# Kernel optimization log

Hardware: AMD Instinct MI355X
Metric: run time of the kernel (lower is better)

## Reference

```python
import jax, jax.numpy as jnp
import numpy as np

N_EMBD = 1024
N_EXPERTS = 8
TOP_K = 2
D_FF = 4 * N_EMBD


def setup_inputs() -> dict:
    key = jax.random.key(0)
    ks = jax.random.split(key, 7)
    s_in = 1.0 / np.sqrt(N_EMBD)
    s_ff = 1.0 / np.sqrt(D_FF)
    return {
        "x": jax.random.normal(ks[0], (2, 2048, N_EMBD), dtype=jnp.float32),
        "Wr": jax.random.normal(ks[1], (N_EMBD, N_EXPERTS), dtype=jnp.float32) * s_in,
        "br": jnp.zeros((N_EXPERTS,), dtype=jnp.float32),
        "W1": jax.random.normal(ks[2], (N_EXPERTS, N_EMBD, D_FF), dtype=jnp.float32) * s_in,
        "b1": jnp.zeros((N_EXPERTS, D_FF), dtype=jnp.float32),
        "W2": jax.random.normal(ks[3], (N_EXPERTS, D_FF, N_EMBD), dtype=jnp.float32) * s_ff,
        "b2": jnp.zeros((N_EXPERTS, N_EMBD), dtype=jnp.float32),
    }


def _moe_forward(x, Wr, br, W1, b1, W2, b2):
    b, t, e = x.shape
    flat_x = x.reshape(-1, e)                      # [T, d]
    T = flat_x.shape[0]
    # --- TopKRouter: logits -> top_k -> sparse softmax over selected experts ---
    logits = flat_x @ Wr + br                      # [T, E]
    top_vals, top_idx = jax.lax.top_k(logits, TOP_K)
    neg_inf = jnp.full_like(logits, -jnp.inf)
    masked = neg_inf.at[jnp.arange(T)[:, None], top_idx].set(top_vals)
    probs = jax.nn.softmax(masked, axis=-1)        # [T, E], zeros outside top-k
    # --- Per-expert FFN, weighted combine (dense weights make this a sum) ---
    out = jnp.zeros_like(flat_x)
    for ei in range(N_EXPERTS):
        h = jax.nn.relu(flat_x @ W1[ei] + b1[ei])  # [T, 4d]
        y = h @ W2[ei] + b2[ei]                    # [T, d]
        out = out + probs[:, ei:ei + 1] * y
    return out.reshape(b, t, e)


def reference(x, Wr, br, W1, b1, W2, b2):
    return _moe_forward(x, Wr, br, W1, b1, W2, b2)
```

## Files before the change

kernel.cpp:

```cpp
#include <hip/hip_runtime.h>
#include <cstdio>
#include <cstdint>

#define TOKS 4096
#define DMODEL 1024
#define DFF 4096
#define NEXP 8

typedef __bf16 bf16_8 __attribute__((ext_vector_type(8)));
typedef float f32x4 __attribute__((ext_vector_type(4)));
typedef __attribute__((address_space(1))) const void* gptr_t;
typedef __attribute__((address_space(3))) void* lptr_t;

__device__ __forceinline__ unsigned short f2bf(float f) {
  unsigned int u = __builtin_bit_cast(unsigned int, f);
  u += 0x7FFFu + ((u >> 16) & 1u);
  return (unsigned short)(u >> 16);
}

__global__ __launch_bounds__(256) void transpose_cast_k(const float* __restrict__ in,
                                                        unsigned short* __restrict__ out,
                                                        int R, int C) {
  __shared__ float tile[64][65];
  const float* inm = in + (size_t)blockIdx.y * R * C;
  unsigned short* outm = out + (size_t)blockIdx.y * R * C;
  int tcn = C >> 6;
  int tr = blockIdx.x / tcn, tc = blockIdx.x % tcn;
  int r0 = tr << 6, c0 = tc << 6;
  int tid = threadIdx.x;
  int lr = tid >> 6, lc = tid & 63;
#pragma unroll
  for (int i = 0; i < 16; ++i)
    tile[lr + 4 * i][lc] = inm[(size_t)(r0 + lr + 4 * i) * C + c0 + lc];
  __syncthreads();
#pragma unroll
  for (int i = 0; i < 8; ++i) {
    int row = (tid >> 5) + i * 8;
    int colu = tid & 31;
    float f0 = tile[colu * 2][row];
    float f1 = tile[colu * 2 + 1][row];
    unsigned int u = (unsigned int)f2bf(f0) | ((unsigned int)f2bf(f1) << 16);
    *(unsigned int*)(outm + (size_t)(c0 + row) * R + r0 + colu * 2) = u;
  }
}

__global__ __launch_bounds__(256) void cast_x_k(const float* __restrict__ x,
                                                unsigned short* __restrict__ xb) {
  int i = blockIdx.x * 256 + threadIdx.x;
  float4 f = ((const float4*)x)[i];
  ushort4 u;
  u.x = f2bf(f.x); u.y = f2bf(f.y); u.z = f2bf(f.z); u.w = f2bf(f.w);
  ((ushort4*)xb)[i] = u;
}

__global__ __launch_bounds__(256) void router_k(const float* __restrict__ x,
                                                const float* __restrict__ Wr,
                                                const float* __restrict__ br,
                                                int* __restrict__ cnt,
                                                int* __restrict__ list,
                                                float* __restrict__ plist) {
  int t = blockIdx.x * 4 + (threadIdx.x >> 6);
  int lane = threadIdx.x & 63;
  float a[NEXP];
#pragma unroll
  for (int e = 0; e < NEXP; ++e) a[e] = 0.f;
  const float* xr = x + (size_t)t * DMODEL;
  for (int i = lane; i < DMODEL; i += 64) {
    float xv = xr[i];
    const float* wr = Wr + (size_t)i * NEXP;
#pragma unroll
    for (int e = 0; e < NEXP; ++e) a[e] += xv * wr[e];
  }
#pragma unroll
  for (int off = 32; off > 0; off >>= 1) {
#pragma unroll
    for (int e = 0; e < NEXP; ++e) a[e] += __shfl_xor(a[e], off);
  }
  if (lane == 0) {
#pragma unroll
    for (int e = 0; e < NEXP; ++e) a[e] += br[e];
    int i0 = 0; float m0 = a[0];
#pragma unroll
    for (int e = 1; e < NEXP; ++e) if (a[e] > m0) { m0 = a[e]; i0 = e; }
    int i1 = -1; float m1 = -1e30f;
#pragma unroll
    for (int e = 0; e < NEXP; ++e) if (e != i0 && a[e] > m1) { m1 = a[e]; i1 = e; }
    float tt = expf(m1 - m0);
    float p0 = 1.f / (1.f + tt);
    float p1 = 1.f - p0;
    int pos0 = atomicAdd(&cnt[i0], 1);
    list[i0 * TOKS + pos0] = t; plist[i0 * TOKS + pos0] = p0;
    int pos1 = atomicAdd(&cnt[i1], 1);
    list[i1 * TOKS + pos1] = t; plist[i1 * TOKS + pos1] = p1;
  }
}

__global__ void offsets_k(const int* __restrict__ cnt, int* __restrict__ off) {
  if (threadIdx.x == 0) {
    int s = 0;
    for (int e = 0; e < NEXP; ++e) { off[e] = s; s += cnt[e]; }
    off[NEXP] = s;
  }
}

template <int MODE, int BM, int BN>
__global__ __launch_bounds__(512, 2) void moe_gemm_k(
    const unsigned short* __restrict__ Abase, const unsigned short* __restrict__ Bbase,
    const float* __restrict__ bias, const int* __restrict__ cnt, const int* __restrict__ off,
    const int* __restrict__ list, const float* __restrict__ plist,
    unsigned short* __restrict__ Hout, float* __restrict__ Out) {
  constexpr int K  = (MODE == 0) ? DMODEL : DFF;
  constexpr int NN = (MODE == 0) ? DFF : DMODEL;
  constexpr int NT = NN / BN;
  constexpr int MT = TOKS / BM;
  constexpr int NWG = NEXP * MT * NT;
  constexpr int CHUNK = NWG / 8;
  constexpr int WMSZ = BM / 2;
  constexpr int WNSZ = BN / 4;
  constexpr int FM = WMSZ / 16;
  constexpr int FN = WNSZ / 16;
  constexpr int RA = BM / 64;
  constexpr int RB = BN / 64;

  const int flat = blockIdx.x + NT * (blockIdx.y + MT * blockIdx.z);
  const int u = (flat & 7) * CHUNK + (flat >> 3);
  const int nt = u % NT;
  const int mt = (u / NT) % MT;
  const int e = u / (NT * MT);

  const int ce = cnt[e];
  const int m0 = mt * BM;
  if (m0 >= ce) return;
  const int rem = ce - m0;
  const int n0 = nt * BN;
  const int oe = off[e];

  __shared__ unsigned short As[2][BM * 64];
  __shared__ unsigned short Bs[2][BN * 64];

  const int tid = threadIdx.x;
  const int lane = tid & 63;
  const int w = tid >> 6;
  const int wm = w >> 2, wn = w & 3;

  const unsigned short* Bm = Bbase + (size_t)e * NN * K;
  const int g = (tid & 7) ^ ((tid >> 3) & 7);

  size_t a_src[RA], b_src[RB];
#pragma unroll
  for (int c = 0; c < RA; ++c) {
    int row = c * 64 + (tid >> 3);
    int rr = row < rem ? row : 0;
    size_t arow;
    if (MODE == 0) arow = (size_t)list[e * TOKS + m0 + rr];
    else           arow = (size_t)(oe + m0 + rr);
    a_src[c] = arow * K + g * 8;
  }
#pragma unroll
  for (int c = 0; c < RB; ++c) {
    int row = c * 64 + (tid >> 3);
    b_src[c] = (size_t)(n0 + row) * K + g * 8;
  }

  f32x4 acc[FM][FN];
#pragma unroll
  for (int i = 0; i < FM; ++i)
#pragma unroll
    for (int j = 0; j < FN; ++j) acc[i][j] = (f32x4){0.f, 0.f, 0.f, 0.f};

  auto STAGE = [&](int buf, int k0) {
#pragma unroll
    for (int c = 0; c < RA; ++c)
      __builtin_amdgcn_global_load_lds((gptr_t)(Abase + a_src[c] + k0),
                                       (lptr_t)&As[buf][(c * 512 + tid) * 8], 16, 0, 0);
#pragma unroll
    for (int c = 0; c < RB; ++c)
      __builtin_amdgcn_global_load_lds((gptr_t)(Bm + b_src[c] + k0),
                                       (lptr_t)&Bs[buf][(c * 512 + tid) * 8], 16, 0, 0);
  };

  auto COMPUTE = [&](int buf) {
#pragma unroll
    for (int kk = 0; kk < 2; ++kk) {
      bf16_8 av[FM], bv[FN];
#pragma unroll
      for (int fm = 0; fm < FM; ++fm) {
        int row = wm * WMSZ + fm * 16 + (lane & 15);
        int slot = row * 8 + ((kk * 4 + (lane >> 4)) ^ (row & 7));
        av[fm] = *(const bf16_8*)&As[buf][slot * 8];
      }
#pragma unroll
      for (int fc = 0; fc < FN; ++fc) {
        int row = wn * WNSZ + fc * 16 + (lane & 15);
        int slot = row * 8 + ((kk * 4 + (lane >> 4)) ^ (row & 7));
        bv[fc] = *(const bf16_8*)&Bs[buf][slot * 8];
      }
#pragma unroll
      for (int fm = 0; fm < FM; ++fm)
#pragma unroll
        for (int fc = 0; fc < FN; ++fc)
          acc[fm][fc] = __builtin_amdgcn_mfma_f32_16x16x32_bf16(av[fm], bv[fc],
                                                                acc[fm][fc], 0, 0, 0);
    }
  };

  constexpr int NSTEP = K / 64;
  STAGE(0, 0);
  __syncthreads();
  int cur = 0;
  for (int t = 0; t < NSTEP - 1; ++t) {
    STAGE(cur ^ 1, (t + 1) * 64);
    COMPUTE(cur);
    __syncthreads();
    cur ^= 1;
  }
  COMPUTE(cur);

  const float* be = bias + (size_t)e * NN + n0;
  if (MODE == 0) {
#pragma unroll
    for (int fm = 0; fm < FM; ++fm) {
#pragma unroll
      for (int j = 0; j < 4; ++j) {
        int row = wm * WMSZ + fm * 16 + (lane >> 4) * 4 + j;
        if (row < rem) {
          unsigned short* hr = Hout + (size_t)(oe + m0 + row) * DFF + n0;
#pragma unroll
          for (int fc = 0; fc < FN; ++fc) {
            int col = wn * WNSZ + fc * 16 + (lane & 15);
            float v = acc[fm][fc][j] + be[col];
            hr[col] = f2bf(fmaxf(v, 0.f));
          }
        }
      }
    }
  } else {
#pragma unroll
    for (int fm = 0; fm < FM; ++fm) {
#pragma unroll
      for (int j = 0; j < 4; ++j) {
        int row = wm * WMSZ + fm * 16 + (lane >> 4) * 4 + j;
        if (row < rem) {
          int tok = list[e * TOKS + m0 + row];
          float p = plist[e * TOKS + m0 + row];
          float* orow = Out + (size_t)tok * DMODEL + n0;
#pragma unroll
          for (int fc = 0; fc < FN; ++fc) {
            int col = wn * WNSZ + fc * 16 + (lane & 15);
            atomicAdd(&orow[col], p * (acc[fm][fc][j] + be[col]));
          }
        }
      }
    }
  }
}

extern "C" void kernel_launch(void* const* d_in, const int* in_sizes, int n_in,
                              void* d_out, int out_size, void* d_ws, size_t ws_size,
                              hipStream_t stream) {
  const float* x  = (const float*)d_in[0];
  const float* Wr = (const float*)d_in[1];
  const float* br = (const float*)d_in[2];
  const float* W1 = (const float*)d_in[3];
  const float* b1 = (const float*)d_in[4];
  const float* W2 = (const float*)d_in[5];
  const float* b2 = (const float*)d_in[6];
  float* out = (float*)d_out;

  const size_t SZ_W = (size_t)NEXP * DMODEL * DFF;
  char* ws = (char*)d_ws;
  size_t o = 0;
  unsigned short* W1t = (unsigned short*)(ws + o); o += SZ_W * 2;
  unsigned short* W2t = (unsigned short*)(ws + o); o += SZ_W * 2;
  unsigned short* xb  = (unsigned short*)(ws + o); o += (size_t)TOKS * DMODEL * 2;
  unsigned short* h   = (unsigned short*)(ws + o); o += (size_t)2 * TOKS * DFF * 2;
  int*   cnt   = (int*)(ws + o);   o += 256;
  int*   offp  = (int*)(ws + o);   o += 256;
  int*   list  = (int*)(ws + o);   o += (size_t)NEXP * TOKS * 4;
  float* plist = (float*)(ws + o); o += (size_t)NEXP * TOKS * 4;
  if (o > ws_size) {
    fprintf(stderr, "kernel_launch: ws too small: need %zu have %zu\n", o, ws_size);
    hipMemsetAsync(d_out, 0, (size_t)out_size * 4, stream);
    return;
  }

  hipMemsetAsync(cnt, 0, 256, stream);
  hipMemsetAsync(d_out, 0, (size_t)out_size * 4, stream);

  transpose_cast_k<<<dim3((DMODEL / 64) * (DFF / 64), NEXP), 256, 0, stream>>>(W1, W1t, DMODEL, DFF);
  transpose_cast_k<<<dim3((DFF / 64) * (DMODEL / 64), NEXP), 256, 0, stream>>>(W2, W2t, DFF, DMODEL);
  cast_x_k<<<TOKS * DMODEL / 4 / 256, 256, 0, stream>>>(x, xb);
  router_k<<<TOKS / 4, 256, 0, stream>>>(x, Wr, br, cnt, list, plist);
  offsets_k<<<1, 64, 0, stream>>>(cnt, offp);
  moe_gemm_k<0, 256, 256><<<dim3(DFF / 256, TOKS / 256, NEXP), 512, 0, stream>>>(
      xb, W1t, b1, cnt, offp, list, plist, h, nullptr);
  moe_gemm_k<1, 256, 128><<<dim3(DMODEL / 128, TOKS / 256, NEXP), 512, 0, stream>>>(
      h, W2t, b2, cnt, offp, list, plist, nullptr, out);
}
```

Measured before the change: 757.7 us.

## Pack weights, activations and hidden into contiguous 64x64 tiles for GEMM loads

Weights are transposed into a blocked layout where each 64x64 bf16 tile is one contiguous 8KB block. Tokens are gathered and cast to bf16 per expert slot in a new gather kernel, replacing the separate x cast. The hidden activations are written back in the same tiled layout. The GEMM no longer does an indirect row gather, and each k-step loads contiguous tiles, which should improve coalescing and TLB locality. The trade-off is that the M grid now spans 2*TOKS slots, so more empty workgroups launch, and the H writes become more scattered 2-byte stores.

```diff
diff --git a/kernel.cpp b/kernel.cpp
--- a/kernel.cpp
+++ b/kernel.cpp
@@ -6,9 +6,11 @@
 #define DMODEL 1024
 #define DFF 4096
 #define NEXP 8
+#define NSLOT (2 * TOKS)
 
 typedef __bf16 bf16_8 __attribute__((ext_vector_type(8)));
 typedef float f32x4 __attribute__((ext_vector_type(4)));
+typedef unsigned short u16x8 __attribute__((ext_vector_type(8)));
 typedef __attribute__((address_space(1))) const void* gptr_t;
 typedef __attribute__((address_space(3))) void* lptr_t;
 
@@ -18,39 +20,37 @@
   return (unsigned short)(u >> 16);
 }
 
-__global__ __launch_bounds__(256) void transpose_cast_k(const float* __restrict__ in,
+__global__ __launch_bounds__(256) void transpose_pack_k(const float* __restrict__ in,
                                                         unsigned short* __restrict__ out,
                                                         int R, int C) {
-  __shared__ float tile[64][65];
-  const float* inm = in + (size_t)blockIdx.y * R * C;
-  unsigned short* outm = out + (size_t)blockIdx.y * R * C;
-  int tcn = C >> 6;
-  int tr = blockIdx.x / tcn, tc = blockIdx.x % tcn;
-  int r0 = tr << 6, c0 = tc << 6;
-  int tid = threadIdx.x;
-  int lr = tid >> 6, lc = tid & 63;
-#pragma unroll
-  for (int i = 0; i < 16; ++i)
-    tile[lr + 4 * i][lc] = inm[(size_t)(r0 + lr + 4 * i) * C + c0 + lc];
+  __shared__ unsigned short tile[64][258];
+  const int e = blockIdx.z;
+  const float* inm = in + (size_t)e * R * C;
+  unsigned short* outm = out + (size_t)e * R * C;
+  const int c0 = blockIdx.x * 256, r0 = blockIdx.y * 64;
+  const int tid = threadIdx.x;
+#pragma unroll
+  for (int i = 0; i < 16; ++i) {
+    int idx = i * 256 + tid;
+    int r = idx >> 6, c4 = idx & 63;
+    float4 f = *(const float4*)&inm[(size_t)(r0 + r) * C + c0 + c4 * 4];
+    tile[r][c4 * 4 + 0] = f2bf(f.x);
+    tile[r][c4 * 4 + 1] = f2bf(f.y);
+    tile[r][c4 * 4 + 2] = f2bf(f.z);
+    tile[r][c4 * 4 + 3] = f2bf(f.w);
+  }
   __syncthreads();
+  const int kp = r0 >> 6, KP = R >> 6;
 #pragma unroll
   for (int i = 0; i < 8; ++i) {
-    int row = (tid >> 5) + i * 8;
-    int colu = tid & 31;
-    float f0 = tile[colu * 2][row];
-    float f1 = tile[colu * 2 + 1][row];
-    unsigned int u = (unsigned int)f2bf(f0) | ((unsigned int)f2bf(f1) << 16);
-    *(unsigned int*)(outm + (size_t)(c0 + row) * R + r0 + colu * 2) = u;
-  }
-}
-
-__global__ __launch_bounds__(256) void cast_x_k(const float* __restrict__ x,
-                                                unsigned short* __restrict__ xb) {
-  int i = blockIdx.x * 256 + threadIdx.x;
-  float4 f = ((const float4*)x)[i];
-  ushort4 u;
-  u.x = f2bf(f.x); u.y = f2bf(f.y); u.z = f2bf(f.z); u.w = f2bf(f.w);
-  ((ushort4*)xb)[i] = u;
+    int ip = i >> 1;
+    int j = (i & 1) * 256 + tid;
+    int nl = j >> 3, k0 = (j & 7) * 8;
+    u16x8 v;
+#pragma unroll
+    for (int jj = 0; jj < 8; ++jj) v[jj] = tile[k0 + jj][ip * 64 + nl];
+    *(u16x8*)(outm + ((size_t)((c0 >> 6) + ip) * KP + kp) * 4096 + nl * 64 + k0) = v;
+  }
 }
 
 __global__ __launch_bounds__(256) void router_k(const float* __restrict__ x,
@@ -103,6 +103,37 @@
   }
 }
 
+__global__ __launch_bounds__(256) void gather_pack_k(const float* __restrict__ x,
+                                                     const int* __restrict__ offp,
+                                                     const int* __restrict__ list,
+                                                     unsigned short* __restrict__ Ap) {
+  __shared__ int soff[NEXP + 1];
+  __shared__ int stok[64];
+  const int sp = blockIdx.x, kp = blockIdx.y;
+  const int tid = threadIdx.x;
+  if (tid < NEXP + 1) soff[tid] = offp[tid];
+  __syncthreads();
+  if (tid < 64) {
+    int s = sp * 64 + tid;
+    int e = 0;
+    while (e < NEXP - 1 && s >= soff[e + 1]) ++e;
+    stok[tid] = list[e * TOKS + (s - soff[e])];
+  }
+  __syncthreads();
+#pragma unroll
+  for (int i = 0; i < 2; ++i) {
+    int j = i * 256 + tid;
+    int nl = j >> 3, g = j & 7;
+    const float* src = x + (size_t)stok[nl] * DMODEL + kp * 64 + g * 8;
+    float4 f0 = *(const float4*)src;
+    float4 f1 = *(const float4*)(src + 4);
+    u16x8 v;
+    v[0] = f2bf(f0.x); v[1] = f2bf(f0.y); v[2] = f2bf(f0.z); v[3] = f2bf(f0.w);
+    v[4] = f2bf(f1.x); v[5] = f2bf(f1.y); v[6] = f2bf(f1.z); v[7] = f2bf(f1.w);
+    *(u16x8*)&Ap[((size_t)sp * (DMODEL / 64) + kp) * 4096 + nl * 64 + g * 8] = v;
+  }
+}
+
 template <int MODE, int BM, int BN>
 __global__ __launch_bounds__(512, 2) void moe_gemm_k(
     const unsigned short* __restrict__ Abase, const unsigned short* __restrict__ Bbase,
@@ -111,8 +142,9 @@
     unsigned short* __restrict__ Hout, float* __restrict__ Out) {
   constexpr int K  = (MODE == 0) ? DMODEL : DFF;
   constexpr int NN = (MODE == 0) ? DFF : DMODEL;
+  constexpr int KP = K >> 6;
   constexpr int NT = NN / BN;
-  constexpr int MT = TOKS / BM;
+  constexpr int MT = NSLOT / BM;
   constexpr int NWG = NEXP * MT * NT;
   constexpr int CHUNK = NWG / 8;
   constexpr int WMSZ = BM / 2;
@@ -151,16 +183,12 @@
   for (int c = 0; c < RA; ++c) {
     int row = c * 64 + (tid >> 3);
     int rr = row < rem ? row : 0;
-    size_t arow;
-    if (MODE == 0) arow = (size_t)list[e * TOKS + m0 + rr];
-    else           arow = (size_t)(oe + m0 + rr);
-    a_src[c] = arow * K + g * 8;
-  }
-#pragma unroll
-  for (int c = 0; c < RB; ++c) {
-    int row = c * 64 + (tid >> 3);
-    b_src[c] = (size_t)(n0 + row) * K + g * 8;
-  }
+    size_t arow = (size_t)(oe + m0 + rr);
+    a_src[c] = (arow >> 6) * ((size_t)KP * 4096) + (arow & 63) * 64 + g * 8;
+  }
+#pragma unroll
+  for (int c = 0; c < RB; ++c)
+    b_src[c] = ((size_t)((n0 >> 6) + c) * KP) * 4096 + (tid >> 3) * 64 + g * 8;
 
   f32x4 acc[FM][FN];
 #pragma unroll
@@ -168,14 +196,15 @@
 #pragma unroll
     for (int j = 0; j < FN; ++j) acc[i][j] = (f32x4){0.f, 0.f, 0.f, 0.f};
 
-  auto STAGE = [&](int buf, int k0) {
+  auto STAGE = [&](int buf, int t) {
+    const size_t ko = (size_t)t * 4096;
 #pragma unroll
     for (int c = 0; c < RA; ++c)
-      __builtin_amdgcn_global_load_lds((gptr_t)(Abase + a_src[c] + k0),
+      __builtin_amdgcn_global_load_lds((gptr_t)(Abase + a_src[c] + ko),
                                        (lptr_t)&As[buf][(c * 512 + tid) * 8], 16, 0, 0);
 #pragma unroll
     for (int c = 0; c < RB; ++c)
-      __builtin_amdgcn_global_load_lds((gptr_t)(Bm + b_src[c] + k0),
+      __builtin_amdgcn_global_load_lds((gptr_t)(Bm + b_src[c] + ko),
                                        (lptr_t)&Bs[buf][(c * 512 + tid) * 8], 16, 0, 0);
   };
 
@@ -209,7 +238,7 @@
   __syncthreads();
   int cur = 0;
   for (int t = 0; t < NSTEP - 1; ++t) {
-    STAGE(cur ^ 1, (t + 1) * 64);
+    STAGE(cur ^ 1, t + 1);
     COMPUTE(cur);
     __syncthreads();
     cur ^= 1;
@@ -224,12 +253,14 @@
       for (int j = 0; j < 4; ++j) {
         int row = wm * WMSZ + fm * 16 + (lane >> 4) * 4 + j;
         if (row < rem) {
-          unsigned short* hr = Hout + (size_t)(oe + m0 + row) * DFF + n0;
+          size_t s = (size_t)(oe + m0 + row);
+          size_t pb = (s >> 6) * ((size_t)(DFF >> 6) * 4096) + (s & 63) * 64;
 #pragma unroll
           for (int fc = 0; fc < FN; ++fc) {
             int col = wn * WNSZ + fc * 16 + (lane & 15);
             float v = acc[fm][fc][j] + be[col];
-            hr[col] = f2bf(fmaxf(v, 0.f));
+            int gc = n0 + col;
+            Hout[pb + (size_t)(gc >> 6) * 4096 + (gc & 63)] = f2bf(fmaxf(v, 0.f));
           }
         }
       }
@@ -272,8 +303,8 @@
   size_t o = 0;
   unsigned short* W1t = (unsigned short*)(ws + o); o += SZ_W * 2;
   unsigned short* W2t = (unsigned short*)(ws + o); o += SZ_W * 2;
-  unsigned short* xb  = (unsigned short*)(ws + o); o += (size_t)TOKS * DMODEL * 2;
-  unsigned short* h   = (unsigned short*)(ws + o); o += (size_t)2 * TOKS * DFF * 2;
+  unsigned short* Ap  = (unsigned short*)(ws + o); o += (size_t)NSLOT * DMODEL * 2;
+  unsigned short* h   = (unsigned short*)(ws + o); o += (size_t)NSLOT * DFF * 2;
   int*   cnt   = (int*)(ws + o);   o += 256;
   int*   offp  = (int*)(ws + o);   o += 256;
   int*   list  = (int*)(ws + o);   o += (size_t)NEXP * TOKS * 4;
@@ -287,13 +318,13 @@
   hipMemsetAsync(cnt, 0, 256, stream);
   hipMemsetAsync(d_out, 0, (size_t)out_size * 4, stream);
 
-  transpose_cast_k<<<dim3((DMODEL / 64) * (DFF / 64), NEXP), 256, 0, stream>>>(W1, W1t, DMODEL, DFF);
-  transpose_cast_k<<<dim3((DFF / 64) * (DMODEL / 64), NEXP), 256, 0, stream>>>(W2, W2t, DFF, DMODEL);
-  cast_x_k<<<TOKS * DMODEL / 4 / 256, 256, 0, stream>>>(x, xb);
+  transpose_pack_k<<<dim3(DFF / 256, DMODEL / 64, NEXP), 256, 0, stream>>>(W1, W1t, DMODEL, DFF);
+  transpose_pack_k<<<dim3(DMODEL / 256, DFF / 64, NEXP), 256, 0, stream>>>(W2, W2t, DFF, DMODEL);
   router_k<<<TOKS / 4, 256, 0, stream>>>(x, Wr, br, cnt, list, plist);
   offsets_k<<<1, 64, 0, stream>>>(cnt, offp);
-  moe_gemm_k<0, 256, 256><<<dim3(DFF / 256, TOKS / 256, NEXP), 512, 0, stream>>>(
-      xb, W1t, b1, cnt, offp, list, plist, h, nullptr);
-  moe_gemm_k<1, 256, 128><<<dim3(DMODEL / 128, TOKS / 256, NEXP), 512, 0, stream>>>(
+  gather_pack_k<<<dim3(NSLOT / 64, DMODEL / 64), 256, 0, stream>>>(x, offp, list, Ap);
+  moe_gemm_k<0, 256, 256><<<dim3(DFF / 256, NSLOT / 256, NEXP), 512, 0, stream>>>(
+      Ap, W1t, b1, cnt, offp, list, plist, h, nullptr);
+  moe_gemm_k<1, 256, 128><<<dim3(DMODEL / 128, NSLOT / 256, NEXP), 512, 0, stream>>>(
       h, W2t, b2, cnt, offp, list, plist, nullptr, out);
 }
```

Result: no change. 745.4 us (-1.6%).
